# Kernel tuning notes

Hardware: AMD Instinct MI355X
Metric: run time of the kernel (lower is better)

The kernel has to match this reference:

```python
import jax, jax.numpy as jnp
import numpy as np

NUM_GRAPHS = 16  # static number of graphs for pooling
BN_EPS = 1e-5


def gat_layer(x, W, a_src, a_dst, src, dst, N, concat):
    # x: (N, Fin), W: (H, Fin, Fout), a_src/a_dst: (H, Fout)
    Wh = jnp.einsum('ni,hio->hno', x, W)                      # (H, N, Fout)
    e_src = jnp.einsum('hno,ho->hn', Wh, a_src)               # (H, N)
    e_dst = jnp.einsum('hno,ho->hn', Wh, a_dst)               # (H, N)
    e = jax.nn.leaky_relu(e_src[:, src] + e_dst[:, dst], 0.2)  # (H, E)
    # edge softmax over incoming edges per dst; torch code starts max at 0
    seg_max = jax.vmap(lambda eh: jax.ops.segment_max(eh, dst, num_segments=N))(e)
    e_max = jnp.maximum(seg_max, 0.0)                         # (H, N)
    exp_e = jnp.exp(e - e_max[:, dst])                        # (H, E)
    exp_sum = jax.vmap(lambda eh: jax.ops.segment_sum(eh, dst, num_segments=N))(exp_e)
    attn = exp_e / (exp_sum[:, dst] + 1e-8)                   # (H, E)
    msgs = attn[:, :, None] * Wh[:, src]                      # (H, E, Fout)
    out = jax.vmap(lambda m: jax.ops.segment_sum(m, dst, num_segments=N))(msgs)  # (H, N, Fout)
    if concat:
        out = jnp.transpose(out, (1, 0, 2)).reshape(N, -1)
    else:
        out = out.mean(axis=0)
    return out, attn


def batchnorm(h, gamma, beta):
    mu = h.mean(axis=0)
    var = h.var(axis=0)
    return (h - mu) / jnp.sqrt(var + BN_EPS) * gamma + beta


def setup_inputs() -> dict:
    key = jax.random.key(0)
    ks = jax.random.split(key, 20)
    N, E = 50000, 400000
    IN, HID, H, NC = 262, 128, 4, 2

    def xavier(k, shape):
        fan_in, fan_out = shape[-2], shape[-1]
        lim = np.sqrt(6.0 / (fan_in + fan_out))
        return jax.random.uniform(k, shape, jnp.float32, -lim, lim)

    x = jax.random.normal(ks[0], (N, IN), jnp.float32)
    edge_index = jax.random.randint(ks[1], (2, E), 0, N, jnp.int64)
    batch = jnp.sort(jax.random.randint(ks[2], (N,), 0, NUM_GRAPHS, jnp.int64))

    return {
        'x': x, 'edge_index': edge_index, 'batch': batch,
        'W1': xavier(ks[3], (H, IN, HID)),
        'a_src1': xavier(ks[4], (H, HID, 1)).squeeze(-1),
        'a_dst1': xavier(ks[5], (H, HID, 1)).squeeze(-1),
        'W2': xavier(ks[6], (1, HID * H, HID)),
        'a_src2': xavier(ks[7], (1, HID, 1)).squeeze(-1),
        'a_dst2': xavier(ks[8], (1, HID, 1)).squeeze(-1),
        'bn1_g': jnp.ones((HID * H,), jnp.float32),
        'bn1_b': jnp.zeros((HID * H,), jnp.float32),
        'bn2_g': jnp.ones((HID,), jnp.float32),
        'bn2_b': jnp.zeros((HID,), jnp.float32),
        'cls_w1': xavier(ks[9], (HID, HID // 2)),
        'cls_b1': jnp.zeros((HID // 2,), jnp.float32),
        'cls_w2': xavier(ks[10], (HID // 2, NC)),
        'cls_b2': jnp.zeros((NC,), jnp.float32),
        'ep_w1': xavier(ks[11], (HID * 2, HID)),
        'ep_b1': jnp.zeros((HID,), jnp.float32),
        'ep_w2': xavier(ks[12], (HID, 1)),
        'ep_b2': jnp.zeros((1,), jnp.float32),
    }


def reference(x, edge_index, batch, W1, a_src1, a_dst1, W2, a_src2, a_dst2,
              bn1_g, bn1_b, bn2_g, bn2_b, cls_w1, cls_b1, cls_w2, cls_b2,
              ep_w1, ep_b1, ep_w2, ep_b2):
    N = x.shape[0]
    src, dst = edge_index[0], edge_index[1]

    h1, _ = gat_layer(x, W1, a_src1, a_dst1, src, dst, N, concat=True)
    h1 = batchnorm(jax.nn.elu(h1), bn1_g, bn1_b)

    h2, attn2 = gat_layer(h1, W2, a_src2, a_dst2, src, dst, N, concat=False)
    h2 = batchnorm(jax.nn.elu(h2), bn2_g, bn2_b)

    # global mean pool over graphs
    sums = jax.ops.segment_sum(h2, batch, num_segments=NUM_GRAPHS)
    counts = jax.ops.segment_sum(jnp.ones((N,), h2.dtype), batch, num_segments=NUM_GRAPHS)
    graph_repr = sums / jnp.clip(counts, 1.0)[:, None]

    logits = jax.nn.relu(graph_repr @ cls_w1 + cls_b1) @ cls_w2 + cls_b2

    edge_feat = jnp.concatenate([h2[src], h2[dst]], axis=1)  # (E, 2*hidden)
    importance = jax.nn.sigmoid(
        (jax.nn.relu(edge_feat @ ep_w1 + ep_b1) @ ep_w2 + ep_b2).squeeze(-1))

    gat_attention = jnp.transpose(attn2, (1, 0))  # (E, 1)
    return logits, h2, importance, gat_attention
```

## Files before the change

### kernel.cpp

```cpp
#include <hip/hip_runtime.h>
#include <hip/hip_bf16.h>
#include <math.h>

typedef __hip_bfloat16 bf16;
typedef __bf16 bf16x8 __attribute__((ext_vector_type(8)));
typedef __bf16 bf16x2v __attribute__((ext_vector_type(2)));
typedef float f32x4 __attribute__((ext_vector_type(4)));

#define NN 50000
#define EE 400000
#define FIN 262
#define KP1 288
#define HID 128
#define NH 4
#define C1 512
#define NGR 16
#define SCAN_NB ((NN + 255) / 256)

__device__ __forceinline__ float b2f(bf16 x){ return __bfloat162float(x); }
__device__ __forceinline__ bf16 f2b(float x){ return __float2bfloat16(x); }
__device__ __forceinline__ float lrelu(float v){ return v >= 0.f ? v : 0.2f * v; }
__device__ __forceinline__ float eluf(float v){ return v > 0.f ? v : expm1f(v); }

__global__ void zero_words(unsigned int* __restrict__ p, int n) {
  int i = blockIdx.x * 256 + threadIdx.x;
  if (i < n) p[i] = 0u;
}

__global__ __launch_bounds__(256)
void gemm_mfma(const bf16* __restrict__ A, const bf16* __restrict__ Bt,
               bf16* __restrict__ C, int M, int K, int Ncols,
               const float* __restrict__ sc, const float* __restrict__ sh) {
  __shared__ __align__(16) __bf16 As[2][128 * 40];
  __shared__ __align__(16) __bf16 Bs[2][128 * 40];
  int bm = blockIdx.y * 128, bn = blockIdx.x * 128;
  int tid = threadIdx.x;
  int wave = tid >> 6, lane = tid & 63;
  int quad = lane >> 4, l16 = lane & 15;
  int wm = (wave >> 1) * 64, wn = (wave & 1) * 64;
  int rowA = (tid * 8) >> 5;
  int colT = (tid * 8) & 31;
  int gm0 = bm + rowA, gm1 = bm + rowA + 64;
  int gn0 = bn + rowA, gn1 = bn + rowA + 64;
  const uint4 zz = {0u, 0u, 0u, 0u};

  f32x4 acc[4][4];
  #pragma unroll
  for (int i = 0; i < 4; ++i)
    #pragma unroll
    for (int j = 0; j < 4; ++j)
      acc[i][j] = (f32x4){0.f, 0.f, 0.f, 0.f};

  uint4 a0, a1, b0, b1;

  auto xf = [&](uint4 v, int kb) -> uint4 {
    if (sc == nullptr) return v;
    bf16x8 a8 = *(bf16x8*)&v;
    float4 c0 = *(const float4*)(sc + kb);
    float4 c1 = *(const float4*)(sc + kb + 4);
    float4 h0 = *(const float4*)(sh + kb);
    float4 h1 = *(const float4*)(sh + kb + 4);
    bf16x8 t8;
    t8[0] = (__bf16)((float)a8[0] * c0.x + h0.x);
    t8[1] = (__bf16)((float)a8[1] * c0.y + h0.y);
    t8[2] = (__bf16)((float)a8[2] * c0.z + h0.z);
    t8[3] = (__bf16)((float)a8[3] * c0.w + h0.w);
    t8[4] = (__bf16)((float)a8[4] * c1.x + h1.x);
    t8[5] = (__bf16)((float)a8[5] * c1.y + h1.y);
    t8[6] = (__bf16)((float)a8[6] * c1.z + h1.z);
    t8[7] = (__bf16)((float)a8[7] * c1.w + h1.w);
    return *(uint4*)&t8;
  };
  auto ld = [&](int k0) {
    a0 = (gm0 < M) ? *(const uint4*)(A + (size_t)gm0 * K + k0 + colT) : zz;
    a1 = (gm1 < M) ? *(const uint4*)(A + (size_t)gm1 * K + k0 + colT) : zz;
    b0 = (gn0 < Ncols) ? *(const uint4*)(Bt + (size_t)gn0 * K + k0 + colT) : zz;
    b1 = (gn1 < Ncols) ? *(const uint4*)(Bt + (size_t)gn1 * K + k0 + colT) : zz;
  };
  auto st = [&](int buf, int k0) {
    *(uint4*)(&As[buf][rowA * 40 + colT])        = xf(a0, k0 + colT);
    *(uint4*)(&As[buf][(rowA + 64) * 40 + colT]) = xf(a1, k0 + colT);
    *(uint4*)(&Bs[buf][rowA * 40 + colT])        = b0;
    *(uint4*)(&Bs[buf][(rowA + 64) * 40 + colT]) = b1;
  };

  int nt = K >> 5;
  ld(0);
  st(0, 0);
  __syncthreads();

  for (int t = 0; t < nt; ++t) {
    int cur = t & 1;
    bool more = (t + 1 < nt);
    if (more) ld((t + 1) << 5);

    bf16x8 af[4], bfr[4];
    #pragma unroll
    for (int i = 0; i < 4; ++i)
      af[i] = *(const bf16x8*)(&As[cur][(wm + i * 16 + l16) * 40 + quad * 8]);
    #pragma unroll
    for (int j = 0; j < 4; ++j)
      bfr[j] = *(const bf16x8*)(&Bs[cur][(wn + j * 16 + l16) * 40 + quad * 8]);
    #pragma unroll
    for (int i = 0; i < 4; ++i)
      #pragma unroll
      for (int j = 0; j < 4; ++j)
        acc[i][j] = __builtin_amdgcn_mfma_f32_16x16x32_bf16(af[i], bfr[j], acc[i][j], 0, 0, 0);

    if (more) st(cur ^ 1, (t + 1) << 5);
    __syncthreads();
  }

  #pragma unroll
  for (int i = 0; i < 4; ++i) {
    #pragma unroll
    for (int r = 0; r < 4; ++r) {
      int gm = bm + wm + i * 16 + quad * 4 + r;
      if (gm >= M) continue;
      #pragma unroll
      for (int j = 0; j < 4; ++j) {
        int gn = bn + wn + j * 16 + l16;
        C[(size_t)gm * Ncols + gn] = f2b(acc[i][j][r]);
      }
    }
  }
}

__global__ void conv_x(const float* __restrict__ x, bf16* __restrict__ xb) {
  int i = blockIdx.x * 256 + threadIdx.x;
  if (i >= NN * KP1) return;
  int row = i / KP1, col = i - row * KP1;
  xb[i] = (col < FIN) ? f2b(x[(size_t)row * FIN + col]) : f2b(0.f);
}
__global__ void prep_b1t(const float* __restrict__ W1, bf16* __restrict__ B1t) {
  int i = blockIdx.x * 256 + threadIdx.x;
  if (i >= C1 * KP1) return;
  int n = i / KP1, k = i - n * KP1;
  int h = n >> 7, o = n & 127;
  B1t[i] = (k < FIN) ? f2b(W1[((size_t)h * FIN + k) * HID + o]) : f2b(0.f);
}
__global__ void prep_b2t(const float* __restrict__ W2, bf16* __restrict__ B2t) {
  int i = blockIdx.x * 256 + threadIdx.x;
  if (i >= HID * C1) return;
  int n = i >> 9, k = i & 511;
  B2t[i] = f2b(W2[(size_t)k * HID + n]);
}
__global__ void prep_bpt(const float* __restrict__ epw1, bf16* __restrict__ BPt) {
  int i = blockIdx.x * 256 + threadIdx.x;
  if (i >= 256 * HID) return;
  int n = i >> 7, k = i & 127;
  float v = (n < 128) ? epw1[(size_t)k * HID + n] : epw1[(size_t)(128 + k) * HID + (n - 128)];
  BPt[i] = f2b(v);
}

__global__ void edot_all(const bf16* __restrict__ Wh1, const float* __restrict__ av,
                         const float* __restrict__ bv, float* __restrict__ es1,
                         float* __restrict__ ed1) {
  int wid = threadIdx.x >> 6, lane = threadIdx.x & 63;
  int n = blockIdx.x * 4 + wid;
  if (n >= NN) return;
  int h = lane >> 4, c16 = lane & 15;
  int fbase = h * HID + c16 * 8;
  bf16x8 r = *(const bf16x8*)(Wh1 + (size_t)n * C1 + fbase);
  float s1 = 0.f, s2 = 0.f;
  #pragma unroll
  for (int j = 0; j < 8; ++j) {
    float rv = (float)r[j];
    s1 += rv * av[fbase + j];
    s2 += rv * bv[fbase + j];
  }
  #pragma unroll
  for (int off = 8; off > 0; off >>= 1) {
    s1 += __shfl_xor(s1, off);
    s2 += __shfl_xor(s2, off);
  }
  if (c16 == 0) { es1[n * 4 + h] = s1; ed1[n * 4 + h] = s2; }
}

__global__ void edot1(const bf16* __restrict__ Wh, const float* __restrict__ av,
                      const float* __restrict__ bv, float* __restrict__ es,
                      float* __restrict__ ed) {
  int wid = threadIdx.x >> 6, lane = threadIdx.x & 63;
  int r = blockIdx.x * 4 + wid;
  if (r >= NN) return;
  const bf16* row = Wh + (size_t)r * HID;
  float w0 = b2f(row[lane]), w1 = b2f(row[lane + 64]);
  float s1 = w0 * av[lane] + w1 * av[lane + 64];
  float s2 = w0 * bv[lane] + w1 * bv[lane + 64];
  #pragma unroll
  for (int off = 32; off > 0; off >>= 1) {
    s1 += __shfl_xor(s1, off);
    s2 += __shfl_xor(s2, off);
  }
  if (lane == 0) { es[r] = s1; ed[r] = s2; }
}

__global__ void count_kernel(const int* __restrict__ dst, int* __restrict__ deg, int E) {
  int e = blockIdx.x * blockDim.x + threadIdx.x;
  if (e >= E) return;
  int d = dst[e];
  if ((unsigned)d < NN) atomicAdd(&deg[d], 1);
}

__global__ void scan_p1(const int* __restrict__ deg, int* __restrict__ bsum) {
  __shared__ int s[256];
  int t = threadIdx.x;
  int i = blockIdx.x * 256 + t;
  s[t] = (i < NN) ? deg[i] : 0;
  __syncthreads();
  #pragma unroll
  for (int off = 128; off > 0; off >>= 1) {
    if (t < off) s[t] += s[t + off];
    __syncthreads();
  }
  if (t == 0) bsum[blockIdx.x] = s[0];
}
__global__ void scan_p2(const int* __restrict__ bsum, int* __restrict__ boff,
                        int* __restrict__ total_out) {
  __shared__ int s[256];
  int t = threadIdx.x;
  s[t] = (t < SCAN_NB) ? bsum[t] : 0;
  __syncthreads();
  if (t == 0) {
    int r = 0;
    for (int i = 0; i < SCAN_NB; ++i) { int v = s[i]; s[i] = r; r += v; }
    total_out[0] = r;
  }
  __syncthreads();
  if (t < SCAN_NB) boff[t] = s[t];
}
__global__ void scan_p3(const int* __restrict__ deg, const int* __restrict__ boff,
                        int* __restrict__ rowptr, int* __restrict__ cursor) {
  __shared__ int s[256];
  int t = threadIdx.x;
  int i = blockIdx.x * 256 + t;
  int v = (i < NN) ? deg[i] : 0;
  s[t] = v;
  __syncthreads();
  #pragma unroll
  for (int off = 1; off < 256; off <<= 1) {
    int add = (t >= off) ? s[t - off] : 0;
    __syncthreads();
    s[t] += add;
    __syncthreads();
  }
  if (i < NN) {
    int pos = boff[blockIdx.x] + s[t] - v;
    rowptr[i] = pos;
    cursor[i] = pos;
  }
}

__global__ void scatter_kernel(const int* __restrict__ src, const int* __restrict__ dst,
                               int* __restrict__ cursor, int* __restrict__ csr_s,
                               int* __restrict__ csr_d, int* __restrict__ csr_e, int E) {
  int e = blockIdx.x * blockDim.x + threadIdx.x;
  if (e >= E) return;
  int d = dst[e];
  if ((unsigned)d >= NN) return;
  int s = src[e]; if ((unsigned)s >= NN) s = 0;
  int p = atomicAdd(&cursor[d], 1);
  if ((unsigned)p < (unsigned)E) { csr_s[p] = s; csr_d[p] = d; csr_e[p] = e; }
}

__global__ __launch_bounds__(256, 6)
void agg1_all(const int* __restrict__ csr_s, const int* __restrict__ rowptr,
              const float* __restrict__ es, const float* __restrict__ ed,
              const bf16* __restrict__ Wh1, bf16* __restrict__ h1) {
  int wid = threadIdx.x >> 6, lane = threadIdx.x & 63;
  int node = blockIdx.x * 4 + wid;
  if (node >= NN) return;
  int b = rowptr[node], e = rowptr[node + 1];
  if (b < 0) b = 0; if (e > EE) e = EE;
  int h = lane >> 4;
  float edh = ed[node * 4 + h];
  float sum = 0.f;
  float acc[8] = {};
  const bf16* W = Wh1 + lane * 8;
  int j = b;
  for (; j + 8 <= e; j += 8) {
    int s_[8];
    #pragma unroll
    for (int i = 0; i < 8; ++i) s_[i] = csr_s[j + i];
    float w[8];
    bf16x8 r[8];
    #pragma unroll
    for (int i = 0; i < 8; ++i) {
      w[i] = es[s_[i] * 4 + h];
      r[i] = *(const bf16x8*)(W + (size_t)s_[i] * C1);
    }
    #pragma unroll
    for (int i = 0; i < 8; ++i) {
      float p = __expf(lrelu(w[i] + edh));
      sum += p;
      #pragma unroll
      for (int k = 0; k < 8; ++k) acc[k] += p * (float)r[i][k];
    }
  }
  if (j + 4 <= e) {
    int s_[4];
    #pragma unroll
    for (int i = 0; i < 4; ++i) s_[i] = csr_s[j + i];
    float w[4];
    bf16x8 r[4];
    #pragma unroll
    for (int i = 0; i < 4; ++i) {
      w[i] = es[s_[i] * 4 + h];
      r[i] = *(const bf16x8*)(W + (size_t)s_[i] * C1);
    }
    #pragma unroll
    for (int i = 0; i < 4; ++i) {
      float p = __expf(lrelu(w[i] + edh));
      sum += p;
      #pragma unroll
      for (int k = 0; k < 8; ++k) acc[k] += p * (float)r[i][k];
    }
    j += 4;
  }
  for (; j < e; ++j) {
    int s0 = csr_s[j];
    float p = __expf(lrelu(es[s0 * 4 + h] + edh));
    bf16x8 r0 = *(const bf16x8*)(W + (size_t)s0 * C1);
    sum += p;
    #pragma unroll
    for (int k = 0; k < 8; ++k) acc[k] += p * (float)r0[k];
  }
  float scale = 1.f / (sum + 1e-8f);
  bf16x8 o;
  #pragma unroll
  for (int k = 0; k < 8; ++k) o[k] = (__bf16)eluf(acc[k] * scale);
  *(bf16x8*)(h1 + (size_t)node * C1 + lane * 8) = o;
}

__global__ __launch_bounds__(256, 8)
void agg2_all(const int* __restrict__ csr_s, const int* __restrict__ rowptr,
              const float* __restrict__ es, const float* __restrict__ ed,
              const bf16* __restrict__ Wh2, bf16* __restrict__ h2p,
              float* __restrict__ invs2) {
  int tid = threadIdx.x;
  int l16 = tid & 15;
  int node = blockIdx.x * 16 + (tid >> 4);
  if (node >= NN) return;
  int b = rowptr[node], e = rowptr[node + 1];
  if (b < 0) b = 0; if (e > EE) e = EE;
  float edn = ed[node];
  float sum = 0.f;
  float acc[8] = {};
  const bf16* W = Wh2 + l16 * 8;
  int j = b;
  for (; j + 4 <= e; j += 4) {
    int s_[4];
    #pragma unroll
    for (int i = 0; i < 4; ++i) s_[i] = csr_s[j + i];
    float w[4];
    bf16x8 r[4];
    #pragma unroll
    for (int i = 0; i < 4; ++i) {
      w[i] = es[s_[i]];
      r[i] = *(const bf16x8*)(W + (size_t)s_[i] * HID);
    }
    #pragma unroll
    for (int i = 0; i < 4; ++i) {
      float p = __expf(lrelu(w[i] + edn));
      sum += p;
      #pragma unroll
      for (int k = 0; k < 8; ++k) acc[k] += p * (float)r[i][k];
    }
  }
  for (; j < e; ++j) {
    int s0 = csr_s[j];
    float p = __expf(lrelu(es[s0] + edn));
    bf16x8 r0 = *(const bf16x8*)(W + (size_t)s0 * HID);
    sum += p;
    #pragma unroll
    for (int k = 0; k < 8; ++k) acc[k] += p * (float)r0[k];
  }
  float scale = 1.f / (sum + 1e-8f);
  bf16x8 o;
  #pragma unroll
  for (int k = 0; k < 8; ++k) o[k] = (__bf16)eluf(acc[k] * scale);
  *(bf16x8*)(h2p + (size_t)node * HID + l16 * 8) = o;
  if (l16 == 0) invs2[node] = scale;
}

__global__ void attn_csr(const int* __restrict__ csr_s, const int* __restrict__ csr_d,
                         const int* __restrict__ csr_e,
                         const float* __restrict__ es2, const float* __restrict__ ed2,
                         const float* __restrict__ invs2, float* __restrict__ out) {
  int j = blockIdx.x * 256 + threadIdx.x;
  if (j >= EE) return;
  int s = csr_s[j]; if ((unsigned)s >= NN) s = 0;
  int d = csr_d[j]; if ((unsigned)d >= NN) d = 0;
  int e = csr_e[j]; if ((unsigned)e >= EE) return;
  float v = lrelu(es2[s] + ed2[d]);
  out[e] = __expf(v) * invs2[d];
}

__global__ void stats_ro(const bf16* __restrict__ X, float* __restrict__ cs,
                         float* __restrict__ cq, int Nrows, int C) {
  int c = threadIdx.x;
  int rpb = (Nrows + gridDim.x - 1) / gridDim.x;
  int r0 = blockIdx.x * rpb, r1 = min(r0 + rpb, Nrows);
  float s = 0.f, s2 = 0.f;
  for (int r = r0; r < r1; ++r) {
    float v = b2f(X[(size_t)r * C + c]);
    s += v; s2 += v * v;
  }
  atomicAdd(&cs[c], s);
  atomicAdd(&cq[c], s2);
}

__global__ void bn_coef(const float* __restrict__ cs, const float* __restrict__ cq,
                        const float* __restrict__ gamma, const float* __restrict__ beta,
                        float* __restrict__ sc, float* __restrict__ sh, int C, float invN) {
  int c = blockIdx.x * 256 + threadIdx.x;
  if (c >= C) return;
  float mu = cs[c] * invN;
  float var = cq[c] * invN - mu * mu;
  float g = rsqrtf(fmaxf(var, 0.f) + 1e-5f) * gamma[c];
  sc[c] = g;
  sh[c] = beta[c] - mu * g;
}

__global__ __launch_bounds__(256)
void poolbn_kernel(const bf16* __restrict__ h2p, const int* __restrict__ batch,
                   const float* __restrict__ sc, const float* __restrict__ sh,
                   float* __restrict__ out_h2, float* __restrict__ pooled) {
  int t = threadIdx.x;
  int f = t & 127, half = t >> 7;
  float scf = sc[f], shf = sh[f];
  int r0 = blockIdx.x * 32;
  int g_cur = -1;
  float acc = 0.f;
  #pragma unroll
  for (int i = 0; i < 16; ++i) {
    int r = r0 + half + 2 * i;
    if (r >= NN) break;
    int g = batch[r]; if ((unsigned)g >= NGR) g = 0;
    float v = b2f(h2p[(size_t)r * HID + f]) * scf + shf;
    out_h2[(size_t)r * HID + f] = v;
    if (g != g_cur) {
      if (g_cur >= 0) atomicAdd(&pooled[g_cur * HID + f], acc);
      g_cur = g; acc = 0.f;
    }
    acc += v;
  }
  if (g_cur >= 0) atomicAdd(&pooled[g_cur * HID + f], acc);
}

__global__ void cls_kernel(const float* __restrict__ pooled, const int* __restrict__ batch,
                           const float* __restrict__ w1, const float* __restrict__ b1,
                           const float* __restrict__ w2, const float* __restrict__ b2,
                           float* __restrict__ out) {
  __shared__ float repr[NGR * HID];
  __shared__ float hid[NGR * 64];
  __shared__ float scnt[NGR];
  int t = threadIdx.x;
  if (t < NGR) {
    int g = t;
    int a = 0, b = NN;
    while (a < b) { int m = (a + b) >> 1; if (batch[m] < g) a = m + 1; else b = m; }
    int lb = a;
    a = 0; b = NN;
    while (a < b) { int m = (a + b) >> 1; if (batch[m] <= g) a = m + 1; else b = m; }
    scnt[t] = (float)(a - lb);
  }
  __syncthreads();
  for (int i = t; i < NGR * HID; i += 128) {
    int g = i >> 7;
    repr[i] = pooled[i] / fmaxf(scnt[g], 1.f);
  }
  __syncthreads();
  for (int i = t; i < NGR * 64; i += 128) {
    int g = i >> 6, j = i & 63;
    float s = b1[j];
    for (int c = 0; c < HID; ++c) s += repr[g * HID + c] * w1[c * 64 + j];
    hid[i] = fmaxf(s, 0.f);
  }
  __syncthreads();
  if (t < NGR * 2) {
    int g = t >> 1, k = t & 1;
    float s = b2[k];
    for (int j = 0; j < 64; ++j) s += hid[g * 64 + j] * w2[j * 2 + k];
    out[t] = s;
  }
}

__global__ __launch_bounds__(256)
void eimp_kernel(const int* __restrict__ csr_s, const int* __restrict__ csr_d,
                 const int* __restrict__ csr_e, const bf16* __restrict__ PQ,
                 const float* __restrict__ b1, const float* __restrict__ w2,
                 const float* __restrict__ b2, float* __restrict__ out) {
  int tid = threadIdx.x;
  int wave = tid >> 6, lane = tid & 63;
  int g = lane >> 4, l16 = lane & 15;
  int slot = blockIdx.x * 16 + wave * 4 + g;
  if (slot >= EE) return;
  int s = csr_s[slot]; if ((unsigned)s >= NN) s = 0;
  int d = csr_d[slot]; if ((unsigned)d >= NN) d = 0;
  int e = csr_e[slot]; if ((unsigned)e >= EE) return;
  bf16x8 p = *(const bf16x8*)(PQ + (size_t)s * 256 + l16 * 8);
  bf16x8 q = *(const bf16x8*)(PQ + (size_t)d * 256 + 128 + l16 * 8);
  float acc = 0.f;
  #pragma unroll
  for (int r = 0; r < 8; ++r) {
    int jj = l16 * 8 + r;
    float hh = (float)p[r] + (float)q[r] + b1[jj];
    hh = fmaxf(hh, 0.f);
    acc += hh * w2[jj];
  }
  #pragma unroll
  for (int off = 8; off > 0; off >>= 1) acc += __shfl_xor(acc, off);
  if (l16 == 0) {
    float z = acc + b2[0];
    out[e] = 1.f / (1.f + expf(-z));
  }
}

extern "C" void kernel_launch(void* const* d_in, const int* in_sizes, int n_in,
                              void* d_out, int out_size, void* d_ws, size_t ws_size,
                              hipStream_t stream) {
  const float* x      = (const float*)d_in[0];
  const int*   ei     = (const int*)d_in[1];
  const int*   batch  = (const int*)d_in[2];
  const float* W1     = (const float*)d_in[3];
  const float* a_src1 = (const float*)d_in[4];
  const float* a_dst1 = (const float*)d_in[5];
  const float* W2     = (const float*)d_in[6];
  const float* a_src2 = (const float*)d_in[7];
  const float* a_dst2 = (const float*)d_in[8];
  const float* bn1_g  = (const float*)d_in[9];
  const float* bn1_b  = (const float*)d_in[10];
  const float* bn2_g  = (const float*)d_in[11];
  const float* bn2_b  = (const float*)d_in[12];
  const float* cls_w1 = (const float*)d_in[13];
  const float* cls_b1 = (const float*)d_in[14];
  const float* cls_w2 = (const float*)d_in[15];
  const float* cls_b2 = (const float*)d_in[16];
  const float* ep_w1  = (const float*)d_in[17];
  const float* ep_b1  = (const float*)d_in[18];
  const float* ep_w2  = (const float*)d_in[19];
  const float* ep_b2  = (const float*)d_in[20];

  const int* srcp = ei;
  const int* dstp = ei + EE;

  char* base = (char*)d_ws;
  bf16* xb   = (bf16*)(base);
  bf16* h1   = (bf16*)(base);
  bf16* Wh1  = (bf16*)(base + 51200000);
  bf16* Wh2  = (bf16*)(base + 51200000);
  bf16* PQ   = (bf16*)(base + 51200000);
  bf16* h2p  = (bf16*)(base + 76800000);
  float* es1   = (float*)(base + 102400000);
  float* ed1   = (float*)(base + 103200000);
  float* es2   = (float*)(base + 104000000);
  float* ed2   = (float*)(base + 104200000);
  int*   deg   = (int*)(base + 104400000);
  float* stats = (float*)(base + 104600000);
  float* cs1 = stats,        *cq1 = stats + 512;
  float* cs2 = stats + 1024, *cq2 = stats + 1152;
  float* pooled = stats + 1280;
  float* sc1   = (float*)(base + 104613376);
  float* sh1   = (float*)(base + 104615424);
  float* sc2   = (float*)(base + 104617472);
  float* sh2   = (float*)(base + 104617984);
  float* invs2 = (float*)(base + 104618496);
  int*   cursor= (int*)(base + 104818496);
  int*   rowptr= (int*)(base + 105018496);
  int*   bsum  = (int*)(base + 105218560);
  int*   boff  = bsum + 256;
  int*   csr_s = (int*)(base + 105220608);
  int*   csr_d = (int*)(base + 106820608);
  int*   csr_e = (int*)(base + 108420608);
  bf16*  B1t   = (bf16*)(base + 110020608);
  bf16*  B2t   = (bf16*)(base + 110315520);
  bf16*  BPt   = (bf16*)(base + 110446592);

  float* out        = (float*)d_out;
  float* out_logits = out;
  float* out_h2     = out + 32;
  float* out_imp    = out + 32 + (size_t)NN * HID;
  float* out_attn   = out_imp + EE;

  zero_words<<<(53344 + 255) / 256, 256, 0, stream>>>((unsigned int*)deg, 53344);

  conv_x<<<(NN * KP1 + 255) / 256, 256, 0, stream>>>(x, xb);
  prep_b1t<<<(C1 * KP1 + 255) / 256, 256, 0, stream>>>(W1, B1t);
  prep_b2t<<<(HID * C1 + 255) / 256, 256, 0, stream>>>(W2, B2t);
  prep_bpt<<<(256 * HID + 255) / 256, 256, 0, stream>>>(ep_w1, BPt);

  count_kernel<<<(EE + 255) / 256, 256, 0, stream>>>(dstp, deg, EE);
  scan_p1<<<SCAN_NB, 256, 0, stream>>>(deg, bsum);
  scan_p2<<<1, 256, 0, stream>>>(bsum, boff, rowptr + NN);
  scan_p3<<<SCAN_NB, 256, 0, stream>>>(deg, boff, rowptr, cursor);
  scatter_kernel<<<(EE + 255) / 256, 256, 0, stream>>>(srcp, dstp, cursor,
                                                       csr_s, csr_d, csr_e, EE);

  dim3 g1(C1 / 128, (NN + 127) / 128);
  gemm_mfma<<<g1, 256, 0, stream>>>(xb, B1t, Wh1, NN, KP1, C1, nullptr, nullptr);
  edot_all<<<(NN + 3) / 4, 256, 0, stream>>>(Wh1, a_src1, a_dst1, es1, ed1);
  agg1_all<<<(NN + 3) / 4, 256, 0, stream>>>(csr_s, rowptr, es1, ed1, Wh1, h1);

  stats_ro<<<400, C1, 0, stream>>>(h1, cs1, cq1, NN, C1);
  bn_coef<<<2, 256, 0, stream>>>(cs1, cq1, bn1_g, bn1_b, sc1, sh1, C1, 1.f / NN);

  dim3 g2(1, (NN + 127) / 128);
  gemm_mfma<<<g2, 256, 0, stream>>>(h1, B2t, Wh2, NN, C1, HID, sc1, sh1);
  edot1<<<(NN + 3) / 4, 256, 0, stream>>>(Wh2, a_src2, a_dst2, es2, ed2);
  agg2_all<<<(NN + 15) / 16, 256, 0, stream>>>(csr_s, rowptr, es2, ed2, Wh2, h2p, invs2);
  attn_csr<<<(EE + 255) / 256, 256, 0, stream>>>(csr_s, csr_d, csr_e, es2, ed2,
                                                 invs2, out_attn);

  stats_ro<<<400, HID, 0, stream>>>(h2p, cs2, cq2, NN, HID);
  bn_coef<<<1, 256, 0, stream>>>(cs2, cq2, bn2_g, bn2_b, sc2, sh2, HID, 1.f / NN);

  poolbn_kernel<<<(NN + 31) / 32, 256, 0, stream>>>(h2p, batch, sc2, sh2, out_h2, pooled);
  cls_kernel<<<1, 128, 0, stream>>>(pooled, batch, cls_w1, cls_b1, cls_w2, cls_b2,
                                    out_logits);

  dim3 gpq(2, (NN + 127) / 128);
  gemm_mfma<<<gpq, 256, 0, stream>>>(h2p, BPt, PQ, NN, HID, 256, sc2, sh2);
  eimp_kernel<<<(EE + 15) / 16, 256, 0, stream>>>(csr_s, csr_d, csr_e, PQ,
                                                  ep_b1, ep_w2, ep_b2, out_imp);
}
```

Before: 607.7 us.

## Swizzle GEMM LDS tiles, merge prep kernels, parallelize scan, fuse attn into agg2

```diff
diff --git a/kernel.cpp b/kernel.cpp
--- a/kernel.cpp
+++ b/kernel.cpp
@@ -31,8 +31,8 @@
 void gemm_mfma(const bf16* __restrict__ A, const bf16* __restrict__ Bt,
                bf16* __restrict__ C, int M, int K, int Ncols,
                const float* __restrict__ sc, const float* __restrict__ sh) {
-  __shared__ __align__(16) __bf16 As[2][128 * 40];
-  __shared__ __align__(16) __bf16 Bs[2][128 * 40];
+  __shared__ __align__(16) __bf16 As[2][128 * 32];
+  __shared__ __align__(16) __bf16 Bs[2][128 * 32];
   int bm = blockIdx.y * 128, bn = blockIdx.x * 128;
   int tid = threadIdx.x;
   int wave = tid >> 6, lane = tid & 63;
@@ -40,6 +40,7 @@
   int wm = (wave >> 1) * 64, wn = (wave & 1) * 64;
   int rowA = (tid * 8) >> 5;
   int colT = (tid * 8) & 31;
+  int swW = ((rowA >> 1) & 3) << 3;
   int gm0 = bm + rowA, gm1 = bm + rowA + 64;
   int gn0 = bn + rowA, gn1 = bn + rowA + 64;
   const uint4 zz = {0u, 0u, 0u, 0u};
@@ -78,10 +79,11 @@
     b1 = (gn1 < Ncols) ? *(const uint4*)(Bt + (size_t)gn1 * K + k0 + colT) : zz;
   };
   auto st = [&](int buf, int k0) {
-    *(uint4*)(&As[buf][rowA * 40 + colT])        = xf(a0, k0 + colT);
-    *(uint4*)(&As[buf][(rowA + 64) * 40 + colT]) = xf(a1, k0 + colT);
-    *(uint4*)(&Bs[buf][rowA * 40 + colT])        = b0;
-    *(uint4*)(&Bs[buf][(rowA + 64) * 40 + colT]) = b1;
+    int cw = colT ^ swW;
+    *(uint4*)(&As[buf][rowA * 32 + cw])        = xf(a0, k0 + colT);
+    *(uint4*)(&As[buf][(rowA + 64) * 32 + cw]) = xf(a1, k0 + colT);
+    *(uint4*)(&Bs[buf][rowA * 32 + cw])        = b0;
+    *(uint4*)(&Bs[buf][(rowA + 64) * 32 + cw]) = b1;
   };
 
   int nt = K >> 5;
@@ -96,11 +98,15 @@
 
     bf16x8 af[4], bfr[4];
     #pragma unroll
-    for (int i = 0; i < 4; ++i)
-      af[i] = *(const bf16x8*)(&As[cur][(wm + i * 16 + l16) * 40 + quad * 8]);
-    #pragma unroll
-    for (int j = 0; j < 4; ++j)
-      bfr[j] = *(const bf16x8*)(&Bs[cur][(wn + j * 16 + l16) * 40 + quad * 8]);
+    for (int i = 0; i < 4; ++i) {
+      int r = wm + i * 16 + l16;
+      af[i] = *(const bf16x8*)(&As[cur][r * 32 + ((quad << 3) ^ (((r >> 1) & 3) << 3))]);
+    }
+    #pragma unroll
+    for (int j = 0; j < 4; ++j) {
+      int r = wn + j * 16 + l16;
+      bfr[j] = *(const bf16x8*)(&Bs[cur][r * 32 + ((quad << 3) ^ (((r >> 1) & 3) << 3))]);
+    }
     #pragma unroll
     for (int i = 0; i < 4; ++i)
       #pragma unroll
@@ -126,31 +132,34 @@
   }
 }
 
-__global__ void conv_x(const float* __restrict__ x, bf16* __restrict__ xb) {
+#define PR0 (NN * KP1)
+#define PR1 (PR0 + C1 * KP1)
+#define PR2 (PR1 + HID * C1)
+#define PR3 (PR2 + 256 * HID)
+__global__ void prep_all(const float* __restrict__ x, const float* __restrict__ W1,
+                         const float* __restrict__ W2, const float* __restrict__ epw1,
+                         bf16* __restrict__ xb, bf16* __restrict__ B1t,
+                         bf16* __restrict__ B2t, bf16* __restrict__ BPt) {
   int i = blockIdx.x * 256 + threadIdx.x;
-  if (i >= NN * KP1) return;
-  int row = i / KP1, col = i - row * KP1;
-  xb[i] = (col < FIN) ? f2b(x[(size_t)row * FIN + col]) : f2b(0.f);
-}
-__global__ void prep_b1t(const float* __restrict__ W1, bf16* __restrict__ B1t) {
-  int i = blockIdx.x * 256 + threadIdx.x;
-  if (i >= C1 * KP1) return;
-  int n = i / KP1, k = i - n * KP1;
-  int h = n >> 7, o = n & 127;
-  B1t[i] = (k < FIN) ? f2b(W1[((size_t)h * FIN + k) * HID + o]) : f2b(0.f);
-}
-__global__ void prep_b2t(const float* __restrict__ W2, bf16* __restrict__ B2t) {
-  int i = blockIdx.x * 256 + threadIdx.x;
-  if (i >= HID * C1) return;
-  int n = i >> 9, k = i & 511;
-  B2t[i] = f2b(W2[(size_t)k * HID + n]);
-}
-__global__ void prep_bpt(const float* __restrict__ epw1, bf16* __restrict__ BPt) {
-  int i = blockIdx.x * 256 + threadIdx.x;
-  if (i >= 256 * HID) return;
-  int n = i >> 7, k = i & 127;
-  float v = (n < 128) ? epw1[(size_t)k * HID + n] : epw1[(size_t)(128 + k) * HID + (n - 128)];
-  BPt[i] = f2b(v);
+  if (i < PR0) {
+    int row = i / KP1, col = i - row * KP1;
+    xb[i] = (col < FIN) ? f2b(x[(size_t)row * FIN + col]) : f2b(0.f);
+  } else if (i < PR1) {
+    int j = i - PR0;
+    int n = j / KP1, k = j - n * KP1;
+    int h = n >> 7, o = n & 127;
+    B1t[j] = (k < FIN) ? f2b(W1[((size_t)h * FIN + k) * HID + o]) : f2b(0.f);
+  } else if (i < PR2) {
+    int j = i - PR1;
+    int n = j >> 9, k = j & 511;
+    B2t[j] = f2b(W2[(size_t)k * HID + n]);
+  } else if (i < PR3) {
+    int j = i - PR2;
+    int n = j >> 7, k = j & 127;
+    float v = (n < 128) ? epw1[(size_t)k * HID + n]
+                        : epw1[(size_t)(128 + k) * HID + (n - 128)];
+    BPt[j] = f2b(v);
+  }
 }
 
 __global__ void edot_all(const bf16* __restrict__ Wh1, const float* __restrict__ av,
@@ -219,15 +228,18 @@
                         int* __restrict__ total_out) {
   __shared__ int s[256];
   int t = threadIdx.x;
-  s[t] = (t < SCAN_NB) ? bsum[t] : 0;
+  int v = (t < SCAN_NB) ? bsum[t] : 0;
+  s[t] = v;
   __syncthreads();
-  if (t == 0) {
-    int r = 0;
-    for (int i = 0; i < SCAN_NB; ++i) { int v = s[i]; s[i] = r; r += v; }
-    total_out[0] = r;
-  }
-  __syncthreads();
-  if (t < SCAN_NB) boff[t] = s[t];
+  #pragma unroll
+  for (int off = 1; off < 256; off <<= 1) {
+    int add = (t >= off) ? s[t - off] : 0;
+    __syncthreads();
+    s[t] += add;
+    __syncthreads();
+  }
+  if (t < SCAN_NB) boff[t] = s[t] - v;
+  if (t == 255) total_out[0] = s[255];
 }
 __global__ void scan_p3(const int* __restrict__ deg, const int* __restrict__ boff,
                         int* __restrict__ rowptr, int* __restrict__ cursor) {
@@ -333,10 +345,11 @@
 }
 
 __global__ __launch_bounds__(256, 8)
-void agg2_all(const int* __restrict__ csr_s, const int* __restrict__ rowptr,
+void agg2_all(const int* __restrict__ csr_s, const int* __restrict__ csr_e,
+              const int* __restrict__ rowptr,
               const float* __restrict__ es, const float* __restrict__ ed,
               const bf16* __restrict__ Wh2, bf16* __restrict__ h2p,
-              float* __restrict__ invs2) {
+              float* __restrict__ out_attn) {
   int tid = threadIdx.x;
   int l16 = tid & 15;
   int node = blockIdx.x * 16 + (tid >> 4);
@@ -380,20 +393,12 @@
   #pragma unroll
   for (int k = 0; k < 8; ++k) o[k] = (__bf16)eluf(acc[k] * scale);
   *(bf16x8*)(h2p + (size_t)node * HID + l16 * 8) = o;
-  if (l16 == 0) invs2[node] = scale;
-}
-
-__global__ void attn_csr(const int* __restrict__ csr_s, const int* __restrict__ csr_d,
-                         const int* __restrict__ csr_e,
-                         const float* __restrict__ es2, const float* __restrict__ ed2,
-                         const float* __restrict__ invs2, float* __restrict__ out) {
-  int j = blockIdx.x * 256 + threadIdx.x;
-  if (j >= EE) return;
-  int s = csr_s[j]; if ((unsigned)s >= NN) s = 0;
-  int d = csr_d[j]; if ((unsigned)d >= NN) d = 0;
-  int e = csr_e[j]; if ((unsigned)e >= EE) return;
-  float v = lrelu(es2[s] + ed2[d]);
-  out[e] = __expf(v) * invs2[d];
+  for (int t = b + l16; t < e; t += 16) {
+    int s0 = csr_s[t];
+    int eid = csr_e[t];
+    float p = __expf(lrelu(es[s0] + edn));
+    if ((unsigned)eid < EE) out_attn[eid] = p * scale;
+  }
 }
 
 __global__ void stats_ro(const bf16* __restrict__ X, float* __restrict__ cs,
@@ -565,7 +570,6 @@
   float* sh1   = (float*)(base + 104615424);
   float* sc2   = (float*)(base + 104617472);
   float* sh2   = (float*)(base + 104617984);
-  float* invs2 = (float*)(base + 104618496);
   int*   cursor= (int*)(base + 104818496);
   int*   rowptr= (int*)(base + 105018496);
   int*   bsum  = (int*)(base + 105218560);
@@ -585,10 +589,7 @@
 
   zero_words<<<(53344 + 255) / 256, 256, 0, stream>>>((unsigned int*)deg, 53344);
 
-  conv_x<<<(NN * KP1 + 255) / 256, 256, 0, stream>>>(x, xb);
-  prep_b1t<<<(C1 * KP1 + 255) / 256, 256, 0, stream>>>(W1, B1t);
-  prep_b2t<<<(HID * C1 + 255) / 256, 256, 0, stream>>>(W2, B2t);
-  prep_bpt<<<(256 * HID + 255) / 256, 256, 0, stream>>>(ep_w1, BPt);
+  prep_all<<<(PR3 + 255) / 256, 256, 0, stream>>>(x, W1, W2, ep_w1, xb, B1t, B2t, BPt);
 
   count_kernel<<<(EE + 255) / 256, 256, 0, stream>>>(dstp, deg, EE);
   scan_p1<<<SCAN_NB, 256, 0, stream>>>(deg, bsum);
@@ -608,9 +609,8 @@
   dim3 g2(1, (NN + 127) / 128);
   gemm_mfma<<<g2, 256, 0, stream>>>(h1, B2t, Wh2, NN, C1, HID, sc1, sh1);
   edot1<<<(NN + 3) / 4, 256, 0, stream>>>(Wh2, a_src2, a_dst2, es2, ed2);
-  agg2_all<<<(NN + 15) / 16, 256, 0, stream>>>(csr_s, rowptr, es2, ed2, Wh2, h2p, invs2);
-  attn_csr<<<(EE + 255) / 256, 256, 0, stream>>>(csr_s, csr_d, csr_e, es2, ed2,
-                                                 invs2, out_attn);
+  agg2_all<<<(NN + 15) / 16, 256, 0, stream>>>(csr_s, csr_e, rowptr, es2, ed2,
+                                               Wh2, h2p, out_attn);
 
   stats_ro<<<400, HID, 0, stream>>>(h2p, cs2, cq2, NN, HID);
   bn_coef<<<1, 256, 0, stream>>>(cs2, cq2, bn2_g, bn2_b, sc2, sh2, HID, 1.f / NN);
```

New measurement: 599.2 us. Within noise of the previous version (-1.4%).
